# Optimization experiments

Measured on AMD Instinct MI355X. Metric: run time of the kernel, lower is better.

The kernel has to match this reference:

```python
import jax, jax.numpy as jnp
import numpy as np

N_NODES = 100000
N_EDGES = 1600000
HIDDEN = 64
N_GRAPHS = 1024
TARGET = 10
ACT_VOCAB = 16
LOC_VOCAB = 1000
TRAVEL_VOCAB = 8
EDGE_DIM = HIDDEN + 3  # edge embed + [duration, tst, tet]
NEG_SLOPE = 0.2  # PyG GATConv default leaky_relu slope


def setup_inputs() -> dict:
    key = jax.random.key(0)
    ks = jax.random.split(key, 20)
    inp = {}
    inp["act"] = jax.random.randint(ks[0], (N_NODES,), 0, ACT_VOCAB)
    inp["location"] = jax.random.randint(ks[1], (N_NODES,), 0, LOC_VOCAB)
    inp["travel"] = jax.random.randint(ks[2], (N_EDGES,), 0, TRAVEL_VOCAB)
    inp["duration"] = jax.random.uniform(ks[3], (N_EDGES,), dtype=jnp.float32)
    inp["tst"] = jax.random.uniform(ks[4], (N_EDGES,), dtype=jnp.float32)
    inp["tet"] = jax.random.uniform(ks[5], (N_EDGES,), dtype=jnp.float32)
    inp["edge_index"] = jax.random.randint(ks[6], (2, N_EDGES), 0, N_NODES)
    inp["batch"] = jnp.sort(jax.random.randint(ks[7], (N_NODES,), 0, N_GRAPHS))
    # learned parameters
    s = 0.05
    inp["emb_act"] = jax.random.normal(ks[8], (ACT_VOCAB, HIDDEN), jnp.float32) * s
    inp["emb_loc"] = jax.random.normal(ks[9], (LOC_VOCAB, HIDDEN), jnp.float32) * s
    inp["emb_travel"] = jax.random.normal(ks[10], (TRAVEL_VOCAB, HIDDEN), jnp.float32) * s
    inp["W_gat"] = jax.random.normal(ks[11], (HIDDEN, HIDDEN), jnp.float32) * s
    inp["att_src"] = jax.random.normal(ks[12], (HIDDEN,), jnp.float32) * s
    inp["att_dst"] = jax.random.normal(ks[13], (HIDDEN,), jnp.float32) * s
    inp["W_edge"] = jax.random.normal(ks[14], (EDGE_DIM, HIDDEN), jnp.float32) * s
    inp["att_edge"] = jax.random.normal(ks[15], (HIDDEN,), jnp.float32) * s
    inp["b_gat"] = jnp.zeros((HIDDEN,), jnp.float32)
    inp["W_fc"] = jax.random.normal(ks[16], (HIDDEN, TARGET), jnp.float32) * s
    inp["b_fc"] = jnp.zeros((TARGET,), jnp.float32)
    return inp


def _forward(act, location, travel, edge_index, batch, duration, tst, tet,
             emb_act, emb_loc, emb_travel, W_gat, att_src, att_dst,
             W_edge, att_edge, b_gat, W_fc, b_fc):
    # MultiTokenEmbedSum: sum of per-feature embeddings -> [N, H]
    x = emb_act[act] + emb_loc[location]
    # edge features: embed(travel) concat [duration, tst, tet] -> [E, H+3]
    x_edge_cont = jnp.stack([duration, tst, tet], axis=1)
    x_edge = jnp.concatenate([emb_travel[travel], x_edge_cont], axis=-1)
    x = jax.nn.relu(x)
    # --- GATConv(H, H), single head, with edge attributes ---
    src, dst = edge_index[0], edge_index[1]
    h = x @ W_gat                                  # [N, H]
    a_src = h @ att_src                            # [N]
    a_dst = h @ att_dst                            # [N]
    he = x_edge @ W_edge                           # [E, H]
    a_edge = he @ att_edge                         # [E]
    alpha = jax.nn.leaky_relu(a_src[src] + a_dst[dst] + a_edge, NEG_SLOPE)
    # segment softmax over incoming edges of each dst node
    m = jax.ops.segment_max(alpha, dst, num_segments=N_NODES)
    e = jnp.exp(alpha - m[dst])
    denom = jax.ops.segment_sum(e, dst, num_segments=N_NODES)
    coef = e / jnp.maximum(denom[dst], 1e-16)      # [E]
    out = jax.ops.segment_sum(coef[:, None] * h[src], dst, num_segments=N_NODES)
    x = jax.nn.relu(out + b_gat)
    # global mean pool over graphs
    sums = jax.ops.segment_sum(x, batch, num_segments=N_GRAPHS)   # [G, H]
    cnt = jax.ops.segment_sum(jnp.ones((N_NODES,), x.dtype), batch, num_segments=N_GRAPHS)
    pooled = sums / jnp.maximum(cnt, 1.0)[:, None]
    # dropout is identity in eval mode
    logits = pooled @ W_fc + b_fc                  # [G, T]
    return jax.nn.log_softmax(logits, axis=1)


def reference(act, location, travel, duration, tst, tet, edge_index, batch,
              emb_act, emb_loc, emb_travel, W_gat, att_src, att_dst,
              W_edge, att_edge, b_gat, W_fc, b_fc):
    return _forward(act, location, travel, edge_index, batch, duration, tst, tet,
                    emb_act, emb_loc, emb_travel, W_gat, att_src, att_dst,
                    W_edge, att_edge, b_gat, W_fc, b_fc)
```

## Files before the change

kernel.cpp:

```cpp
#include <hip/hip_runtime.h>
#include <math.h>

#define HIDDEN 64
#define TARGET 10
#define BKSH 9
#define NBKMAX 256

static __device__ __forceinline__ unsigned short f2bf(float f) {
    unsigned int u = __float_as_uint(f);
    u = (u + 0x7fffu + ((u >> 16) & 1u)) >> 16;
    return (unsigned short)u;
}
static __device__ __forceinline__ float bf2f(unsigned short v) {
    return __uint_as_float((unsigned int)v << 16);
}

__global__ __launch_bounds__(256) void k_nodes(
        const int* __restrict__ act, const int* __restrict__ loc,
        const float* __restrict__ emb_act,
        const float* __restrict__ emb_loc,
        const float* __restrict__ W_gat,
        const float* __restrict__ att_src,
        const float* __restrict__ att_dst,
        unsigned short* __restrict__ hb,
        float* __restrict__ a_src, float* __restrict__ a_dst,
        int N) {
    __shared__ float xs[64][68];
    __shared__ float Wl[64][68];
    __shared__ int acts[64], locs[64];
    int tid = threadIdx.x;
    int base = blockIdx.x * 64;

    for (int i = tid; i < 4096; i += 256) Wl[i >> 6][i & 63] = W_gat[i];
    if (tid < 64) {
        int n = base + tid;
        acts[tid] = (n < N) ? act[n] : 0;
        locs[tid] = (n < N) ? loc[n] : 0;
    }
    __syncthreads();

    for (int i = tid; i < 1024; i += 256) {
        int r = i >> 4, k4 = i & 15;
        int n = base + r;
        float4 v = make_float4(0.f, 0.f, 0.f, 0.f);
        if (n < N) {
            float4 a = ((const float4*)emb_act)[acts[r] * 16 + k4];
            float4 b = ((const float4*)emb_loc)[locs[r] * 16 + k4];
            v.x = fmaxf(a.x + b.x, 0.f);
            v.y = fmaxf(a.y + b.y, 0.f);
            v.z = fmaxf(a.z + b.z, 0.f);
            v.w = fmaxf(a.w + b.w, 0.f);
        }
        *(float4*)&xs[r][k4 * 4] = v;
    }
    __syncthreads();

    int tx = tid & 15, ty = tid >> 4;
    float acc[4][4];
#pragma unroll
    for (int i = 0; i < 4; i++)
#pragma unroll
        for (int j = 0; j < 4; j++) acc[i][j] = 0.f;

#pragma unroll 4
    for (int k4 = 0; k4 < 16; k4++) {
        float4 xv[4], wv[4];
#pragma unroll
        for (int i = 0; i < 4; i++) xv[i] = *(const float4*)&xs[ty * 4 + i][k4 * 4];
#pragma unroll
        for (int kk = 0; kk < 4; kk++) wv[kk] = *(const float4*)&Wl[k4 * 4 + kk][tx * 4];
#pragma unroll
        for (int i = 0; i < 4; i++) {
            float xk0 = xv[i].x, xk1 = xv[i].y, xk2 = xv[i].z, xk3 = xv[i].w;
            acc[i][0] += xk0 * wv[0].x + xk1 * wv[1].x + xk2 * wv[2].x + xk3 * wv[3].x;
            acc[i][1] += xk0 * wv[0].y + xk1 * wv[1].y + xk2 * wv[2].y + xk3 * wv[3].y;
            acc[i][2] += xk0 * wv[0].z + xk1 * wv[1].z + xk2 * wv[2].z + xk3 * wv[3].z;
            acc[i][3] += xk0 * wv[0].w + xk1 * wv[1].w + xk2 * wv[2].w + xk3 * wv[3].w;
        }
    }

#pragma unroll
    for (int i = 0; i < 4; i++) {
        int n = base + ty * 4 + i;
        if (n < N) {
            ushort4 hv;
            hv.x = f2bf(acc[i][0]); hv.y = f2bf(acc[i][1]);
            hv.z = f2bf(acc[i][2]); hv.w = f2bf(acc[i][3]);
            *(ushort4*)&hb[(size_t)n * 64 + tx * 4] = hv;
        }
    }

    float4 as4 = ((const float4*)att_src)[tx];
    float4 ad4 = ((const float4*)att_dst)[tx];
    float ps[4], pd[4];
#pragma unroll
    for (int i = 0; i < 4; i++) {
        ps[i] = acc[i][0] * as4.x + acc[i][1] * as4.y + acc[i][2] * as4.z + acc[i][3] * as4.w;
        pd[i] = acc[i][0] * ad4.x + acc[i][1] * ad4.y + acc[i][2] * ad4.z + acc[i][3] * ad4.w;
    }
#pragma unroll
    for (int off = 1; off < 16; off <<= 1) {
#pragma unroll
        for (int i = 0; i < 4; i++) {
            ps[i] += __shfl_xor(ps[i], off, 64);
            pd[i] += __shfl_xor(pd[i], off, 64);
        }
    }
    if (tx == 0) {
#pragma unroll
        for (int i = 0; i < 4; i++) {
            int n = base + ty * 4 + i;
            if (n < N) { a_src[n] = ps[i]; a_dst[n] = pd[i]; }
        }
    }
}

__global__ __launch_bounds__(256) void k_binA(
        const int* __restrict__ src, const int* __restrict__ dst,
        const int* __restrict__ travel,
        const float* __restrict__ dur,
        const float* __restrict__ tst,
        const float* __restrict__ tet,
        const float* __restrict__ a_src,
        const float* __restrict__ a_dst,
        const float* __restrict__ W_edge,
        const float* __restrict__ att_edge,
        const float* __restrict__ emb_travel,
        int* __restrict__ bcur,
        int2* __restrict__ epk, int E, int CAP) {
    __shared__ float we_s[67];
    __shared__ float ttbl[8];
    __shared__ float c012[3];
    __shared__ int cnt[NBKMAX];
    __shared__ int gb[NBKMAX];
    int tid = threadIdx.x;
    if (tid < 67) {
        float s = 0.f;
        for (int j = 0; j < 64; j++) s += W_edge[tid * 64 + j] * att_edge[j];
        we_s[tid] = s;
    }
    if (tid < NBKMAX) cnt[tid] = 0;
    __syncthreads();
    if (tid < 8) {
        float s = 0.f;
        for (int k = 0; k < 64; k++) s += emb_travel[tid * 64 + k] * we_s[k];
        ttbl[tid] = s;
    }
    if (tid == 64) { c012[0] = we_s[64]; c012[1] = we_s[65]; c012[2] = we_s[66]; }
    __syncthreads();
    float c0 = c012[0], c1 = c012[1], c2 = c012[2];

    int base = blockIdx.x * 2048 + tid;
    int rx[8], bks[8];
    float rv[8];
    bool ok[8];
#pragma unroll
    for (int j = 0; j < 8; j++) {
        int e = base + j * 256;
        ok[j] = e < E;
        if (ok[j]) {
            int s = src[e], d = dst[e];
            float al = a_src[s] + a_dst[d] + ttbl[travel[e]]
                     + c0 * dur[e] + c1 * tst[e] + c2 * tet[e];
            al = al > 0.f ? al : 0.2f * al;
            rv[j] = __expf(al);
            rx[j] = s | ((d & 511) << 20);
            bks[j] = d >> BKSH;
            atomicAdd(&cnt[bks[j]], 1);
        }
    }
    __syncthreads();
    if (tid < NBKMAX) {
        int c = cnt[tid];
        gb[tid] = c ? atomicAdd(&bcur[tid], c) : 0;
        cnt[tid] = 0;
    }
    __syncthreads();
#pragma unroll
    for (int j = 0; j < 8; j++) {
        if (ok[j]) {
            int slot = atomicAdd(&cnt[bks[j]], 1);
            int2 p;
            p.x = rx[j];
            p.y = __float_as_int(rv[j]);
            epk[(size_t)bks[j] * CAP + gb[bks[j]] + slot] = p;
        }
    }
}

__global__ __launch_bounds__(256) void k_binB(
        const int2* __restrict__ epk,
        const int* __restrict__ bcur,
        int2* __restrict__ epk2,
        int2* __restrict__ rowse, int N, int CAP) {
    __shared__ int cnt[512];
    __shared__ int cur[512];
    int tid = threadIdx.x;
    int bk = blockIdx.x;
    int n0 = bk << BKSH;
    int cnt0 = bcur[bk];
    size_t base = (size_t)bk * CAP;

    for (int j = tid; j < 512; j += 256) cnt[j] = 0;
    __syncthreads();
    const int* epx = (const int*)epk;
    for (int i = tid; i < cnt0; i += 256)
        atomicAdd(&cnt[(epx[(base + i) * 2] >> 20) & 511], 1);
    __syncthreads();
    if (tid < 64) {
        int carry = 0;
#pragma unroll
        for (int c = 0; c < 8; c++) {
            int idx = c * 64 + tid;
            int v = cnt[idx];
            int s = v;
#pragma unroll
            for (int off = 1; off < 64; off <<= 1) {
                int t = __shfl_up(s, off, 64);
                if (tid >= off) s += t;
            }
            int excl = carry + s - v;
            cur[idx] = excl;
            int n = n0 + idx;
            if (n < N) rowse[n] = make_int2((int)base + excl, (int)base + excl + v);
            carry += __shfl(s, 63, 64);
        }
    }
    __syncthreads();
    for (int i = tid; i < cnt0; i += 256) {
        int2 p = epk[base + i];
        int dl = (p.x >> 20) & 511;
        int pos = atomicAdd(&cur[dl], 1);
        epk2[base + pos] = p;
    }
}

__global__ __launch_bounds__(256) void k_gather(
        const int2* __restrict__ epk,
        const int2* __restrict__ rowse,
        const uint4* __restrict__ hbq,
        const float4* __restrict__ bg4,
        const int* __restrict__ batch,
        float* __restrict__ pooled_sums, int N) {
    int lane = threadIdx.x & 63;
    int wid = (blockIdx.x * blockDim.x + threadIdx.x) >> 6;
    int nw = (gridDim.x * blockDim.x) >> 6;
    int chunk = (N + nw - 1) / nw;
    int n0 = wid * chunk;
    if (n0 >= N) return;
    int n1 = n0 + chunk;
    if (n1 > N) n1 = N;
    int grp = lane >> 3;
    int sub = lane & 7;
    float4 b0 = bg4[sub * 2], b1 = bg4[sub * 2 + 1];
    int curg = -1;
    float p0 = 0.f, p1 = 0.f, p2 = 0.f, p3 = 0.f;
    float p4 = 0.f, p5 = 0.f, p6 = 0.f, p7 = 0.f;
    for (int n = n0; n < n1; n++) {
        int g = batch[n];
        if (g != curg) {
            if (curg >= 0 && grp == 0) {
                float* ps = &pooled_sums[(size_t)curg * 64 + sub * 8];
                unsafeAtomicAdd(ps + 0, p0);
                unsafeAtomicAdd(ps + 1, p1);
                unsafeAtomicAdd(ps + 2, p2);
                unsafeAtomicAdd(ps + 3, p3);
                unsafeAtomicAdd(ps + 4, p4);
                unsafeAtomicAdd(ps + 5, p5);
                unsafeAtomicAdd(ps + 6, p6);
                unsafeAtomicAdd(ps + 7, p7);
            }
            p0 = p1 = p2 = p3 = p4 = p5 = p6 = p7 = 0.f;
            curg = g;
        }
        int2 se = rowse[n];
        float a0 = 0.f, a1 = 0.f, a2 = 0.f, a3 = 0.f;
        float a4 = 0.f, a5 = 0.f, a6 = 0.f, a7 = 0.f, dv = 0.f;
        for (int e0 = se.x; e0 < se.y; e0 += 8) {
            int e = e0 + grp;
            if (e < se.y) {
                int2 p = epk[e];
                float ev = __int_as_float(p.y);
                int sidx = p.x & 0xFFFFF;
                uint4 hu = hbq[(size_t)sidx * 8 + sub];
                a0 += ev * bf2f((unsigned short)(hu.x));
                a1 += ev * bf2f((unsigned short)(hu.x >> 16));
                a2 += ev * bf2f((unsigned short)(hu.y));
                a3 += ev * bf2f((unsigned short)(hu.y >> 16));
                a4 += ev * bf2f((unsigned short)(hu.z));
                a5 += ev * bf2f((unsigned short)(hu.z >> 16));
                a6 += ev * bf2f((unsigned short)(hu.w));
                a7 += ev * bf2f((unsigned short)(hu.w >> 16));
                dv += ev;
            }
        }
#pragma unroll
        for (int off = 8; off < 64; off <<= 1) {
            a0 += __shfl_xor(a0, off, 64);
            a1 += __shfl_xor(a1, off, 64);
            a2 += __shfl_xor(a2, off, 64);
            a3 += __shfl_xor(a3, off, 64);
            a4 += __shfl_xor(a4, off, 64);
            a5 += __shfl_xor(a5, off, 64);
            a6 += __shfl_xor(a6, off, 64);
            a7 += __shfl_xor(a7, off, 64);
            dv += __shfl_xor(dv, off, 64);
        }
        float dn = dv > 1e-16f ? dv : 1e-16f;
        float inv = 1.f / dn;
        p0 += fmaxf(a0 * inv + b0.x, 0.f);
        p1 += fmaxf(a1 * inv + b0.y, 0.f);
        p2 += fmaxf(a2 * inv + b0.z, 0.f);
        p3 += fmaxf(a3 * inv + b0.w, 0.f);
        p4 += fmaxf(a4 * inv + b1.x, 0.f);
        p5 += fmaxf(a5 * inv + b1.y, 0.f);
        p6 += fmaxf(a6 * inv + b1.z, 0.f);
        p7 += fmaxf(a7 * inv + b1.w, 0.f);
    }
    if (curg >= 0 && grp == 0) {
        float* ps = &pooled_sums[(size_t)curg * 64 + sub * 8];
        unsafeAtomicAdd(ps + 0, p0);
        unsafeAtomicAdd(ps + 1, p1);
        unsafeAtomicAdd(ps + 2, p2);
        unsafeAtomicAdd(ps + 3, p3);
        unsafeAtomicAdd(ps + 4, p4);
        unsafeAtomicAdd(ps + 5, p5);
        unsafeAtomicAdd(ps + 6, p6);
        unsafeAtomicAdd(ps + 7, p7);
    }
}

__global__ void k_fc(const float* __restrict__ pooled_sums,
                     const int* __restrict__ batch, int N,
                     const float* __restrict__ W_fc,
                     const float* __restrict__ b_fc,
                     float* __restrict__ out, int G) {
    int lane = threadIdx.x & 63;
    int wid = (blockIdx.x * blockDim.x + threadIdx.x) >> 6;
    int nw = (gridDim.x * blockDim.x) >> 6;
    for (int g = wid; g < G; g += nw) {
        int lo = 0, hi = N;
        while (lo < hi) { int mid = (lo + hi) >> 1; if (batch[mid] < g) lo = mid + 1; else hi = mid; }
        int start = lo;
        hi = N;
        while (lo < hi) { int mid = (lo + hi) >> 1; if (batch[mid] < g + 1) lo = mid + 1; else hi = mid; }
        float cnt = (float)(lo - start);
        float inv = 1.f / (cnt > 1.f ? cnt : 1.f);
        float p = pooled_sums[(size_t)g * 64 + lane] * inv;
        float logit[TARGET];
#pragma unroll
        for (int t = 0; t < TARGET; t++) {
            float v = p * W_fc[lane * TARGET + t];
#pragma unroll
            for (int o = 32; o > 0; o >>= 1) v += __shfl_xor(v, o, 64);
            logit[t] = v + b_fc[t];
        }
        float m = logit[0];
#pragma unroll
        for (int t = 1; t < TARGET; t++) m = fmaxf(m, logit[t]);
        float se = 0.f;
#pragma unroll
        for (int t = 0; t < TARGET; t++) se += expf(logit[t] - m);
        float lse = m + logf(se);
#pragma unroll
        for (int t = 0; t < TARGET; t++)
            if (lane == t) out[g * TARGET + t] = logit[t] - lse;
    }
}

extern "C" void kernel_launch(void* const* d_in, const int* in_sizes, int n_in,
                              void* d_out, int out_size, void* d_ws, size_t ws_size,
                              hipStream_t stream) {
    const int*   act        = (const int*)d_in[0];
    const int*   loc        = (const int*)d_in[1];
    const int*   travel     = (const int*)d_in[2];
    const float* dur        = (const float*)d_in[3];
    const float* tst        = (const float*)d_in[4];
    const float* tet        = (const float*)d_in[5];
    const int*   ei         = (const int*)d_in[6];
    const int*   batch      = (const int*)d_in[7];
    const float* emb_act    = (const float*)d_in[8];
    const float* emb_loc    = (const float*)d_in[9];
    const float* emb_travel = (const float*)d_in[10];
    const float* W_gat      = (const float*)d_in[11];
    const float* att_src    = (const float*)d_in[12];
    const float* att_dst    = (const float*)d_in[13];
    const float* W_edge     = (const float*)d_in[14];
    const float* att_edge   = (const float*)d_in[15];
    const float* b_gat      = (const float*)d_in[16];
    const float* W_fc       = (const float*)d_in[17];
    const float* b_fc       = (const float*)d_in[18];
    float* out = (float*)d_out;

    int N = in_sizes[0];
    int E = in_sizes[2];
    int G = out_size / TARGET;
    int NBK = (N + 511) >> BKSH;
    int CAP = (((E + NBK - 1) / NBK) + 4096 + 15) & ~15;

    float* ws = (float*)d_ws;
    size_t off = 0;
    unsigned short* hb = (unsigned short*)(ws + off); off += (size_t)N * 32;
    float* a_src    = ws + off; off += N;
    float* a_dst    = ws + off; off += N;
    int*   bcur     = (int*)(ws + off); off += NBKMAX;
    if (off & 1) off++;
    int2*  rowse    = (int2*)(ws + off); off += (size_t)N * 2;
    int2*  epk      = (int2*)(ws + off); off += (size_t)NBK * CAP * 2;
    int2*  epk2     = (int2*)(ws + off); off += (size_t)NBK * CAP * 2;
    float* pooled   = ws + off; off += (size_t)G * 64;

    hipMemsetAsync(bcur, 0, (size_t)NBKMAX * sizeof(int), stream);
    hipMemsetAsync(pooled, 0, (size_t)G * 64 * sizeof(float), stream);

    k_nodes<<<(N + 63) / 64, 256, 0, stream>>>(act, loc, emb_act, emb_loc, W_gat,
                                               att_src, att_dst, hb, a_src, a_dst, N);
    k_binA<<<(E + 2047) / 2048, 256, 0, stream>>>(ei, ei + E, travel, dur, tst, tet,
                                                  a_src, a_dst, W_edge, att_edge,
                                                  emb_travel, bcur, epk, E, CAP);
    k_binB<<<NBK, 256, 0, stream>>>(epk, bcur, epk2, rowse, N, CAP);
    k_gather<<<2048, 256, 0, stream>>>(epk2, rowse,
                                       (const uint4*)hb, (const float4*)b_gat,
                                       batch, pooled, N);
    k_fc<<<256, 256, 0, stream>>>(pooled, batch, N, W_fc, b_fc, out, G);
}
```

Baseline: 167.1 us.

## Double per-block edge count in binning, unroll gather by two, merge memsets

The binning kernel now handles 16 edges per thread (4096 per block), which halves the block count and the per-block setup and global bucket atomics. The gather loop processes two edges per lane per iteration, using clamped indices and zero masks instead of a branch, so more independent loads are in flight. The bucket-counter and pooled-sum buffers are made adjacent so a single memset clears both. The cost is higher register pressure in both kernels and wasted loads on the masked tail edges.

Result: no change. 167.7 us (+0.4%).

```diff
diff --git a/kernel.cpp b/kernel.cpp
--- a/kernel.cpp
+++ b/kernel.cpp
@@ -150,12 +150,12 @@
     __syncthreads();
     float c0 = c012[0], c1 = c012[1], c2 = c012[2];
 
-    int base = blockIdx.x * 2048 + tid;
-    int rx[8], bks[8];
-    float rv[8];
-    bool ok[8];
-#pragma unroll
-    for (int j = 0; j < 8; j++) {
+    int base = blockIdx.x * 4096 + tid;
+    int rx[16], bks[16];
+    float rv[16];
+    bool ok[16];
+#pragma unroll
+    for (int j = 0; j < 16; j++) {
         int e = base + j * 256;
         ok[j] = e < E;
         if (ok[j]) {
@@ -177,7 +177,7 @@
     }
     __syncthreads();
 #pragma unroll
-    for (int j = 0; j < 8; j++) {
+    for (int j = 0; j < 16; j++) {
         if (ok[j]) {
             int slot = atomicAdd(&cnt[bks[j]], 1);
             int2 p;
@@ -276,23 +276,37 @@
         int2 se = rowse[n];
         float a0 = 0.f, a1 = 0.f, a2 = 0.f, a3 = 0.f;
         float a4 = 0.f, a5 = 0.f, a6 = 0.f, a7 = 0.f, dv = 0.f;
-        for (int e0 = se.x; e0 < se.y; e0 += 8) {
-            int e = e0 + grp;
-            if (e < se.y) {
-                int2 p = epk[e];
-                float ev = __int_as_float(p.y);
-                int sidx = p.x & 0xFFFFF;
-                uint4 hu = hbq[(size_t)sidx * 8 + sub];
-                a0 += ev * bf2f((unsigned short)(hu.x));
-                a1 += ev * bf2f((unsigned short)(hu.x >> 16));
-                a2 += ev * bf2f((unsigned short)(hu.y));
-                a3 += ev * bf2f((unsigned short)(hu.y >> 16));
-                a4 += ev * bf2f((unsigned short)(hu.z));
-                a5 += ev * bf2f((unsigned short)(hu.z >> 16));
-                a6 += ev * bf2f((unsigned short)(hu.w));
-                a7 += ev * bf2f((unsigned short)(hu.w >> 16));
-                dv += ev;
-            }
+        int lastE = se.y - 1;
+        for (int e0 = se.x; e0 < se.y; e0 += 16) {
+            int ea = e0 + grp;
+            int eb = ea + 8;
+            float ma = ea <= lastE ? 1.f : 0.f;
+            float mb = eb <= lastE ? 1.f : 0.f;
+            ea = ea <= lastE ? ea : lastE;
+            eb = eb <= lastE ? eb : lastE;
+            int2 pa = epk[ea];
+            int2 pb = epk[eb];
+            float eva = __int_as_float(pa.y) * ma;
+            float evb = __int_as_float(pb.y) * mb;
+            uint4 hua = hbq[(size_t)(pa.x & 0xFFFFF) * 8 + sub];
+            uint4 hub = hbq[(size_t)(pb.x & 0xFFFFF) * 8 + sub];
+            a0 += eva * bf2f((unsigned short)(hua.x));
+            a1 += eva * bf2f((unsigned short)(hua.x >> 16));
+            a2 += eva * bf2f((unsigned short)(hua.y));
+            a3 += eva * bf2f((unsigned short)(hua.y >> 16));
+            a4 += eva * bf2f((unsigned short)(hua.z));
+            a5 += eva * bf2f((unsigned short)(hua.z >> 16));
+            a6 += eva * bf2f((unsigned short)(hua.w));
+            a7 += eva * bf2f((unsigned short)(hua.w >> 16));
+            a0 += evb * bf2f((unsigned short)(hub.x));
+            a1 += evb * bf2f((unsigned short)(hub.x >> 16));
+            a2 += evb * bf2f((unsigned short)(hub.y));
+            a3 += evb * bf2f((unsigned short)(hub.y >> 16));
+            a4 += evb * bf2f((unsigned short)(hub.z));
+            a5 += evb * bf2f((unsigned short)(hub.z >> 16));
+            a6 += evb * bf2f((unsigned short)(hub.w));
+            a7 += evb * bf2f((unsigned short)(hub.w >> 16));
+            dv += eva + evb;
         }
 #pragma unroll
         for (int off = 8; off < 64; off <<= 1) {
@@ -404,18 +418,17 @@
     float* a_src    = ws + off; off += N;
     float* a_dst    = ws + off; off += N;
     int*   bcur     = (int*)(ws + off); off += NBKMAX;
+    float* pooled   = ws + off; off += (size_t)G * 64;
     if (off & 1) off++;
     int2*  rowse    = (int2*)(ws + off); off += (size_t)N * 2;
     int2*  epk      = (int2*)(ws + off); off += (size_t)NBK * CAP * 2;
     int2*  epk2     = (int2*)(ws + off); off += (size_t)NBK * CAP * 2;
-    float* pooled   = ws + off; off += (size_t)G * 64;
-
-    hipMemsetAsync(bcur, 0, (size_t)NBKMAX * sizeof(int), stream);
-    hipMemsetAsync(pooled, 0, (size_t)G * 64 * sizeof(float), stream);
+
+    hipMemsetAsync(bcur, 0, (NBKMAX + (size_t)G * 64) * sizeof(float), stream);
 
     k_nodes<<<(N + 63) / 64, 256, 0, stream>>>(act, loc, emb_act, emb_loc, W_gat,
                                                att_src, att_dst, hb, a_src, a_dst, N);
-    k_binA<<<(E + 2047) / 2048, 256, 0, stream>>>(ei, ei + E, travel, dur, tst, tet,
+    k_binA<<<(E + 4095) / 4096, 256, 0, stream>>>(ei, ei + E, travel, dur, tst, tet,
                                                   a_src, a_dst, W_edge, att_edge,
                                                   emb_travel, bcur, epk, E, CAP);
     k_binB<<<NBK, 256, 0, stream>>>(epk, bcur, epk2, rowse, N, CAP);
```
